# Performance work log

Hardware: AMD Instinct MI355X
Metric: run time of the kernel (lower is better)

The kernel has to match this reference:

```python
import jax, jax.numpy as jnp
import numpy as np


def setup_inputs() -> dict:
    key = jax.random.key(0)
    k1, k2 = jax.random.split(key)
    latents = jax.random.normal(k1, (32, 1024, 64), dtype=jnp.float32)
    codebook = jax.random.normal(k2, (8192, 64), dtype=jnp.float32)
    return {"latents": latents, "codebook": codebook}


def reference(latents, codebook):
    # Faithful to: cdist(latents_flat, codebook) -> argmin(dim=1) -> reshape(B, L)
    B, L, D = latents.shape
    x = latents.reshape(-1, D)                         # (N, D)
    x2 = jnp.sum(x * x, axis=1, keepdims=True)         # (N, 1)
    c2 = jnp.sum(codebook * codebook, axis=1)          # (K,)
    # (N, K) distance matrix, then argmin reduction
    d2 = x2 - 2.0 * (x @ codebook.T) + c2[None, :]
    indices = jnp.argmin(d2, axis=1)                   # (N,)
    return indices.reshape(B, L)
```

## Files before the change

### kernel.cpp

```cpp
#include <hip/hip_runtime.h>
#include <stdint.h>


#define N_TOTAL 32768
#define K_CODES 8192
#define EPS_GAP 0.008f

typedef __attribute__((ext_vector_type(16))) float  floatx16;
typedef __attribute__((ext_vector_type(8)))  __bf16 bf16x8;

#define O_C2    0u
#define O_CBSW  32768u
#define O_PS1   2129920u
#define O_PS2   2654208u
#define O_PI1   3178496u
#define O_CNT   3702784u
#define O_LIST  3703040u
#define O_SLOT  3834112u
#define WS_NEED 4096256u

__device__ __forceinline__ unsigned int fkey(float s) {
    unsigned int u = __float_as_uint(s);
    return (u & 0x80000000u) ? ~u : (u | 0x80000000u);
}

__device__ __forceinline__ void load_lds16(const void* g, void* l) {
    __builtin_amdgcn_global_load_lds(
        (const __attribute__((address_space(1))) unsigned int*)g,
        (__attribute__((address_space(3))) unsigned int*)l, 16, 0, 0);
}

__global__ __launch_bounds__(256) void vq_prep(
    const float4* __restrict__ cb, uint4* __restrict__ cbSw,
    float* __restrict__ c2, int* __restrict__ cnt) {
    __shared__ float red[256];
    const int m = threadIdx.x & 31, g = threadIdx.x >> 5;
    const int rb = blockIdx.x;
    if (rb == 0 && threadIdx.x == 0) *cnt = 0;
    float4 a = cb[(size_t)(rb * 32 + m) * 16 + g * 2];
    float4 b = cb[(size_t)(rb * 32 + m) * 16 + g * 2 + 1];
    float x[8] = {a.x, a.y, a.z, a.w, b.x, b.y, b.z, b.w};
    bf16x8 hv, lv;
    float ss = 0.f;
#pragma unroll
    for (int i = 0; i < 8; ++i) {
        float v  = x[i];
        __bf16 hb = (__bf16)v;
        float r  = v - (float)hb;
        hv[i] = hb;
        lv[i] = (__bf16)r;
        ss += v * v;
    }
    cbSw[(size_t)rb * 512 + g * 32 + m]       = __builtin_bit_cast(uint4, hv);
    cbSw[(size_t)rb * 512 + (8 + g) * 32 + m] = __builtin_bit_cast(uint4, lv);
    red[threadIdx.x] = ss;
    __syncthreads();
    if (threadIdx.x < 32) {
        float s = 0.f;
#pragma unroll
        for (int gg = 0; gg < 8; ++gg) s += red[threadIdx.x + 32 * gg];
        c2[rb * 32 + threadIdx.x] = s;
    }
}

__global__ __launch_bounds__(256, 2) void vq_mfma(
    const float4* __restrict__ lat, const uint4* __restrict__ cbSw,
    const float* __restrict__ c2,
    float* __restrict__ pS1, float* __restrict__ pS2, int* __restrict__ pI1) {
    __shared__ uint4 Bs[2][1024];
    const int tid = threadIdx.x;
    const int wr = tid >> 6, lane = tid & 63;
    const int m = lane & 31, h = lane >> 5;

    const int q = blockIdx.x * 128 + wr * 32 + m;
    bf16x8 aH[4], aL[4];
#pragma unroll
    for (int c = 0; c < 4; ++c) {
        float4 v0 = lat[(size_t)q * 16 + c * 4 + h * 2];
        float4 v1 = lat[(size_t)q * 16 + c * 4 + h * 2 + 1];
        float x[8] = {v0.x, v0.y, v0.z, v0.w, v1.x, v1.y, v1.z, v1.w};
#pragma unroll
        for (int j = 0; j < 8; ++j) {
            float v  = x[j];
            __bf16 hb = (__bf16)v;
            aH[c][j] = hb;
            aL[c][j] = (__bf16)(v - (float)hb);
        }
    }

    float t1[16], t2[16]; int i1[16];
#pragma unroll
    for (int r = 0; r < 16; ++r) { t1[r] = -3e38f; t2[r] = -3e38f; i1[r] = 0; }

    const int kBase = blockIdx.y * 2048;
    const uint4* srcBase = cbSw + ((size_t)(kBase >> 5) << 9);
    const int dOff = wr * 64 + lane;

#pragma unroll
    for (int i = 0; i < 4; ++i)
        load_lds16(&srcBase[256 * i + dOff], &Bs[0][wr * 64 + 256 * i]);
    float c2n0 = c2[kBase + m];
    float c2n1 = c2[kBase + 32 + m];
    __syncthreads();
    float nn0 = -0.5f * c2n0;
    float nn1 = -0.5f * c2n1;

    for (int stage = 0; stage < 32; ++stage) {
        const int cur = stage & 1;
        if (stage + 1 < 32) {
            const uint4* sp = srcBase + (size_t)(stage + 1) * 1024;
#pragma unroll
            for (int i = 0; i < 4; ++i)
                load_lds16(&sp[256 * i + dOff], &Bs[cur ^ 1][wr * 64 + 256 * i]);
            c2n0 = c2[kBase + (stage + 1) * 64 + m];
            c2n1 = c2[kBase + (stage + 1) * 64 + 32 + m];
        }

#pragma unroll
        for (int kb = 0; kb < 2; ++kb) {
            const int col = kBase + stage * 64 + kb * 32 + m;
            const float nn = kb ? nn1 : nn0;
            floatx16 acc;
#pragma unroll
            for (int r = 0; r < 16; ++r) acc[r] = nn;
#pragma unroll
            for (int c = 0; c < 4; ++c) {
                bf16x8 bH = __builtin_bit_cast(bf16x8, Bs[cur][kb * 512 + (c * 2 + h) * 32 + m]);
                bf16x8 bL = __builtin_bit_cast(bf16x8, Bs[cur][kb * 512 + (8 + c * 2 + h) * 32 + m]);
                acc = __builtin_amdgcn_mfma_f32_32x32x16_bf16(aH[c], bH, acc, 0, 0, 0);
                acc = __builtin_amdgcn_mfma_f32_32x32x16_bf16(aL[c], bH, acc, 0, 0, 0);
                acc = __builtin_amdgcn_mfma_f32_32x32x16_bf16(aH[c], bL, acc, 0, 0, 0);
            }
#pragma unroll
            for (int r = 0; r < 16; ++r) {
                float a = acc[r];
                bool gt = a > t1[r];
                t2[r] = __builtin_amdgcn_fmed3f(a, t1[r], t2[r]);
                t1[r] = fmaxf(t1[r], a);
                i1[r] = gt ? col : i1[r];
            }
        }

        __syncthreads();
        nn0 = -0.5f * c2n0;
        nn1 = -0.5f * c2n1;
    }

#pragma unroll
    for (int mask = 1; mask <= 16; mask <<= 1) {
#pragma unroll
        for (int r = 0; r < 16; ++r) {
            float o1 = __shfl_xor(t1[r], mask);
            float o2 = __shfl_xor(t2[r], mask);
            int   oi = __shfl_xor(i1[r], mask);
            float n2 = fmaxf(fmaxf(t2[r], o2), fminf(t1[r], o1));
            bool take = (o1 > t1[r]) || (o1 == t1[r] && oi < i1[r]);
            t1[r] = take ? o1 : t1[r];
            i1[r] = take ? oi : i1[r];
            t2[r] = n2;
        }
    }

    if (m == 0) {
        const int qb = blockIdx.x * 128 + wr * 32;
        const int o0 = blockIdx.y * N_TOTAL;
#pragma unroll
        for (int r = 0; r < 16; ++r) {
            int row = (r & 3) + 8 * (r >> 2) + 4 * h;
            int qq = qb + row;
            pS1[o0 + qq] = -2.f * t1[r];
            pS2[o0 + qq] = -2.f * t2[r];
            pI1[o0 + qq] = i1[r];
        }
    }
}

__global__ void vq_merge4(const float* __restrict__ pS1, const float* __restrict__ pS2,
                          const int* __restrict__ pI1, int* __restrict__ out,
                          int* __restrict__ cnt, int* __restrict__ list,
                          unsigned long long* __restrict__ slot) {
    int q = blockIdx.x * 256 + threadIdx.x;
    float g1 = 3e38f, g2 = 3e38f;
    int   gi = 0x7FFFFFFF;
#pragma unroll
    for (int p = 0; p < 4; ++p) {
        float s1p = pS1[p * N_TOTAL + q];
        float s2p = pS2[p * N_TOTAL + q];
        int   i1p = pI1[p * N_TOTAL + q];
        bool take = (s1p < g1) || (s1p == g1 && i1p < gi);
        g2 = fminf(g2, fminf(s2p, take ? g1 : s1p));
        if (take) { g1 = s1p; gi = i1p; }
    }
    out[q] = gi;
    if (g2 - g1 < EPS_GAP) {
        int e = atomicAdd(cnt, 1);
        list[e] = q;
        slot[e] = 0xFFFFFFFFFFFFFFFFull;
    }
}

__global__ __launch_bounds__(256) void vq_exact2(
    const float4* __restrict__ lat, const float4* __restrict__ cb,
    const float* __restrict__ c2, const int* __restrict__ cnt,
    const int* __restrict__ list, unsigned long long* __restrict__ slot) {
    __shared__ float qv[4][64];
    const int n = *cnt;
    const int totalChunks = n * 8;
    const int wInB = threadIdx.x >> 6;
    const int lane = threadIdx.x & 63;

    for (int base = blockIdx.x * 4; base < totalChunks; base += gridDim.x * 4) {
        const int c = base + wInB;
        const bool act = c < totalChunks;
        int e = 0, q = 0, kb = 0;
        if (act) { e = c >> 3; q = list[e]; kb = (c & 7) << 10; }
        __syncthreads();
        if (act && lane < 16) {
            float4 v = lat[(size_t)q * 16 + lane];
            *(float4*)&qv[wInB][lane * 4] = v;
        }
        __syncthreads();
        if (act) {
            float best = 3e38f; int bi = 0;
#pragma unroll 2
            for (int i = 0; i < 16; ++i) {
                const int k = kb + i * 64 + lane;
                float dot = 0.f;
#pragma unroll
                for (int d4 = 0; d4 < 16; ++d4) {
                    float4 cv = cb[(size_t)k * 16 + d4];
                    dot += qv[wInB][d4 * 4 + 0] * cv.x + qv[wInB][d4 * 4 + 1] * cv.y
                         + qv[wInB][d4 * 4 + 2] * cv.z + qv[wInB][d4 * 4 + 3] * cv.w;
                }
                float s = c2[k] - 2.f * dot;
                if (s < best) { best = s; bi = k; }
            }
            unsigned long long p = ((unsigned long long)fkey(best) << 32) | (unsigned)bi;
#pragma unroll
            for (int mask = 1; mask <= 32; mask <<= 1) {
                unsigned long long o = __shfl_xor(p, mask);
                p = o < p ? o : p;
            }
            if (lane == 0) atomicMin(&slot[e], p);
        }
    }
}

__global__ void vq_write(const int* __restrict__ cnt, const int* __restrict__ list,
                         const unsigned long long* __restrict__ slot,
                         int* __restrict__ out) {
    int t = blockIdx.x * 256 + threadIdx.x;
    if (t < *cnt) out[list[t]] = (int)(slot[t] & 0xFFFFFFFFull);
}

#define BM 128
#define BN 128
#define PAD 68

__global__ void vq_norms_fb(const float4* __restrict__ cb, float* __restrict__ c2) {
    int t = blockIdx.x * 256 + threadIdx.x;
    int r = t >> 2, p = t & 3;
    float s = 0.f;
#pragma unroll
    for (int i = 0; i < 4; ++i) {
        float4 v = cb[r * 16 + p * 4 + i];
        s += v.x * v.x + v.y * v.y + v.z * v.z + v.w * v.w;
    }
    s += __shfl_xor(s, 1);
    s += __shfl_xor(s, 2);
    if (p == 0) c2[r] = s;
}

__global__ __launch_bounds__(256) void vq_fp32(
    const float4* __restrict__ lat, const float4* __restrict__ cb,
    const float* __restrict__ c2, int ktPer,
    int* __restrict__ outIdx, float* __restrict__ partS, int* __restrict__ partI,
    int writePartial) {
    __shared__ float As[BM][PAD];
    __shared__ float Bsf[BN][PAD];
    __shared__ float c2s[BN];
    const int tid = threadIdx.x;
    const int tx = tid & 15;
    const int ty = tid >> 4;
    const int nBase = blockIdx.x * BM;
    const int kt0 = blockIdx.y * ktPer;
    const int ktN = kt0 + ktPer;
#pragma unroll
    for (int r = 0; r < 8; ++r) {
        int f = tid + 256 * r;
        int mm = f >> 4, d4 = f & 15;
        float4 v = lat[(size_t)(nBase + mm) * 16 + d4];
        *(float4*)&As[mm][d4 * 4] = v;
    }
    float best[8]; int bidx[8];
#pragma unroll
    for (int ii = 0; ii < 8; ++ii) { best[ii] = 3e38f; bidx[ii] = 0; }
    for (int kt = kt0; kt < ktN; ++kt) {
        const int kbase = kt * BN;
        __syncthreads();
#pragma unroll
        for (int r = 0; r < 8; ++r) {
            int f = tid + 256 * r;
            int k = f >> 4, d4 = f & 15;
            float4 v = cb[(size_t)(kbase + k) * 16 + d4];
            *(float4*)&Bsf[k][d4 * 4] = v;
        }
        if (tid < BN) c2s[tid] = c2[kbase + tid];
        __syncthreads();
        float acc[8][8];
#pragma unroll
        for (int ii = 0; ii < 8; ++ii)
#pragma unroll
            for (int jj = 0; jj < 8; ++jj) acc[ii][jj] = 0.f;
#pragma unroll 4
        for (int d4 = 0; d4 < 16; ++d4) {
            float4 a[8], b[8];
#pragma unroll
            for (int ii = 0; ii < 8; ++ii) a[ii] = *(const float4*)&As[tx + 16 * ii][d4 * 4];
#pragma unroll
            for (int jj = 0; jj < 8; ++jj) b[jj] = *(const float4*)&Bsf[ty + 16 * jj][d4 * 4];
#pragma unroll
            for (int ii = 0; ii < 8; ++ii)
#pragma unroll
                for (int jj = 0; jj < 8; ++jj)
                    acc[ii][jj] += a[ii].x * b[jj].x + a[ii].y * b[jj].y
                                 + a[ii].z * b[jj].z + a[ii].w * b[jj].w;
        }
#pragma unroll
        for (int jj = 0; jj < 8; ++jj) {
            int k = kbase + ty + 16 * jj;
            float cc = c2s[ty + 16 * jj];
#pragma unroll
            for (int ii = 0; ii < 8; ++ii) {
                float s = cc - 2.f * acc[ii][jj];
                if (s < best[ii]) { best[ii] = s; bidx[ii] = k; }
            }
        }
    }
    __syncthreads();
    float* redS = &As[0][0];
    int*   redI = (int*)&Bsf[0][0];
#pragma unroll
    for (int ii = 0; ii < 8; ++ii) {
        int mm = tx + 16 * ii;
        redS[ty * BM + mm] = best[ii];
        redI[ty * BM + mm] = bidx[ii];
    }
    __syncthreads();
    if (tid < BM) {
        int mm = tid;
        float bs = redS[mm]; int bi = redI[mm];
#pragma unroll
        for (int t = 1; t < 16; ++t) {
            float s = redS[t * BM + mm]; int i = redI[t * BM + mm];
            if (s < bs || (s == bs && i < bi)) { bs = s; bi = i; }
        }
        int n = nBase + mm;
        if (writePartial) { partS[blockIdx.y * N_TOTAL + n] = bs; partI[blockIdx.y * N_TOTAL + n] = bi; }
        else outIdx[n] = bi;
    }
}

__global__ void vq_merge_fb(const float* __restrict__ partS, const int* __restrict__ partI,
                            int* __restrict__ out) {
    int n = blockIdx.x * 256 + threadIdx.x;
    float s0 = partS[n], s1 = partS[N_TOTAL + n];
    int   i0 = partI[n], i1 = partI[N_TOTAL + n];
    out[n] = (s1 < s0) ? i1 : i0;
}

extern "C" void kernel_launch(void* const* d_in, const int* in_sizes, int n_in,
                              void* d_out, int out_size, void* d_ws, size_t ws_size,
                              hipStream_t stream) {
    const float4* lat = (const float4*)d_in[0];
    const float4* cb  = (const float4*)d_in[1];
    int* out = (int*)d_out;
    char* ws = (char*)d_ws;

    if (ws_size >= WS_NEED) {
        float* c2   = (float*)(ws + O_C2);
        uint4* cbSw = (uint4*)(ws + O_CBSW);
        float* pS1  = (float*)(ws + O_PS1);
        float* pS2  = (float*)(ws + O_PS2);
        int*   pI1  = (int*)(ws + O_PI1);
        int*   cnt  = (int*)(ws + O_CNT);
        int*   list = (int*)(ws + O_LIST);
        unsigned long long* slot = (unsigned long long*)(ws + O_SLOT);

        vq_prep<<<256, 256, 0, stream>>>(cb, cbSw, c2, cnt);
        vq_mfma<<<dim3(256, 4), 256, 0, stream>>>(lat, cbSw, c2, pS1, pS2, pI1);
        vq_merge4<<<128, 256, 0, stream>>>(pS1, pS2, pI1, out, cnt, list, slot);
        vq_exact2<<<1024, 256, 0, stream>>>(lat, cb, c2, cnt, list, slot);
        vq_write<<<128, 256, 0, stream>>>(cnt, list, slot, out);
    } else {
        float* c2 = (float*)ws;
        vq_norms_fb<<<128, 256, 0, stream>>>(cb, c2);
        const size_t needSplit = 32768u + 2u * N_TOTAL * 4u + 2u * N_TOTAL * 4u + 64u;
        if (ws_size >= needSplit) {
            float* partS = (float*)(ws + 32768);
            int*   partI = (int*)(ws + 32768 + 2 * N_TOTAL * 4);
            dim3 grid(N_TOTAL / BM, 2);
            vq_fp32<<<grid, 256, 0, stream>>>(lat, cb, c2, (K_CODES / BN) / 2, out, partS, partI, 1);
            vq_merge_fb<<<N_TOTAL / 256, 256, 0, stream>>>(partS, partI, out);
        } else {
            dim3 grid(N_TOTAL / BM, 1);
            vq_fp32<<<grid, 256, 0, stream>>>(lat, cb, c2, K_CODES / BN, out, nullptr, nullptr, 0);
        }
    }
}
```

Before: 223.3 us.

## Triple-buffer codebook LDS tiles and preload squared norms into shared memory

Replaces the double-buffered codebook staging with a three-buffer ring. Loads run two stages ahead, and each iteration uses a single barrier gated by a partial vmcnt wait instead of a trailing full __syncthreads. The per-block slice of codebook squared norms is loaded once into LDS, so the loop no longer issues global loads for it. The goal is to hide global-to-LDS latency behind the MFMA work and cut synchronisation stalls. The cost is more LDS per block, which may limit occupancy, plus redundant reloads of the last stage at the tail.

```diff
diff --git a/kernel.cpp b/kernel.cpp
--- a/kernel.cpp
+++ b/kernel.cpp
@@ -67,7 +67,8 @@
     const float4* __restrict__ lat, const uint4* __restrict__ cbSw,
     const float* __restrict__ c2,
     float* __restrict__ pS1, float* __restrict__ pS2, int* __restrict__ pI1) {
-    __shared__ uint4 Bs[2][1024];
+    __shared__ uint4 Bs[3][1024];
+    __shared__ float c2s[2048];
     const int tid = threadIdx.x;
     const int wr = tid >> 6, lane = tid & 63;
     const int m = lane & 31, h = lane >> 5;
@@ -96,25 +97,40 @@
     const uint4* srcBase = cbSw + ((size_t)(kBase >> 5) << 9);
     const int dOff = wr * 64 + lane;
 
+    {
+        const float4* c2p = (const float4*)(c2 + kBase);
+        float4 f0 = c2p[tid * 2];
+        float4 f1 = c2p[tid * 2 + 1];
+        *(float4*)&c2s[tid * 8]     = f0;
+        *(float4*)&c2s[tid * 8 + 4] = f1;
+    }
+    __syncthreads();
+
 #pragma unroll
     for (int i = 0; i < 4; ++i)
         load_lds16(&srcBase[256 * i + dOff], &Bs[0][wr * 64 + 256 * i]);
-    float c2n0 = c2[kBase + m];
-    float c2n1 = c2[kBase + 32 + m];
-    __syncthreads();
-    float nn0 = -0.5f * c2n0;
-    float nn1 = -0.5f * c2n1;
-
+#pragma unroll
+    for (int i = 0; i < 4; ++i)
+        load_lds16(&srcBase[1024 + 256 * i + dOff], &Bs[1][wr * 64 + 256 * i]);
+
+    int cur = 0;
     for (int stage = 0; stage < 32; ++stage) {
-        const int cur = stage & 1;
-        if (stage + 1 < 32) {
-            const uint4* sp = srcBase + (size_t)(stage + 1) * 1024;
+        __builtin_amdgcn_sched_barrier(0);
+        asm volatile("s_waitcnt vmcnt(4)" ::: "memory");
+        __builtin_amdgcn_s_barrier();
+        __builtin_amdgcn_sched_barrier(0);
+
+        {
+            int nb = cur + 2; if (nb >= 3) nb -= 3;
+            const int nxt = (stage + 2 < 32) ? (stage + 2) : 31;
+            const uint4* sp = srcBase + (size_t)nxt * 1024;
 #pragma unroll
             for (int i = 0; i < 4; ++i)
-                load_lds16(&sp[256 * i + dOff], &Bs[cur ^ 1][wr * 64 + 256 * i]);
-            c2n0 = c2[kBase + (stage + 1) * 64 + m];
-            c2n1 = c2[kBase + (stage + 1) * 64 + 32 + m];
-        }
+                load_lds16(&sp[256 * i + dOff], &Bs[nb][wr * 64 + 256 * i]);
+        }
+
+        float nn0 = -0.5f * c2s[stage * 64 + m];
+        float nn1 = -0.5f * c2s[stage * 64 + 32 + m];
 
 #pragma unroll
         for (int kb = 0; kb < 2; ++kb) {
@@ -140,11 +156,9 @@
                 i1[r] = gt ? col : i1[r];
             }
         }
-
-        __syncthreads();
-        nn0 = -0.5f * c2n0;
-        nn1 = -0.5f * c2n1;
-    }
+        if (++cur == 3) cur = 0;
+    }
+    asm volatile("s_waitcnt vmcnt(0)" ::: "memory");
 
 #pragma unroll
     for (int mask = 1; mask <= 16; mask <<= 1) {
```

Result: no change. 226.9 us (+1.6%).

## Switch codebook search MFMA to 16x16x32 tiles with LDS-staged norms

Applied to the files above, without the earlier changes.

Restructures the main distance kernel from 32x32x16 MFMA tiles (128 queries per block) to 16x16x32 tiles (64 queries per block), which doubles the grid and cuts per-thread accumulator and top-2 register state. The block's codebook norms are now staged once into shared memory instead of being reloaded from global memory every stage. The kernel also raises wave priority around the MFMA section and requests three blocks per CU instead of two. The trade-off is that each block reuses the codebook tile across fewer queries, so total LDS and codebook traffic doubles in exchange for higher occupancy and less register pressure.

```diff
diff --git a/kernel.cpp b/kernel.cpp
--- a/kernel.cpp
+++ b/kernel.cpp
@@ -6,6 +6,7 @@
 #define K_CODES 8192
 #define EPS_GAP 0.008f
 
+typedef __attribute__((ext_vector_type(4)))  float  floatx4;
 typedef __attribute__((ext_vector_type(16))) float  floatx16;
 typedef __attribute__((ext_vector_type(8)))  __bf16 bf16x8;
 
@@ -63,21 +64,22 @@
     }
 }
 
-__global__ __launch_bounds__(256, 2) void vq_mfma(
+__global__ __launch_bounds__(256, 3) void vq_mfma(
     const float4* __restrict__ lat, const uint4* __restrict__ cbSw,
     const float* __restrict__ c2,
     float* __restrict__ pS1, float* __restrict__ pS2, int* __restrict__ pI1) {
     __shared__ uint4 Bs[2][1024];
+    __shared__ float c2s[2048];
     const int tid = threadIdx.x;
     const int wr = tid >> 6, lane = tid & 63;
-    const int m = lane & 31, h = lane >> 5;
-
-    const int q = blockIdx.x * 128 + wr * 32 + m;
-    bf16x8 aH[4], aL[4];
-#pragma unroll
-    for (int c = 0; c < 4; ++c) {
-        float4 v0 = lat[(size_t)q * 16 + c * 4 + h * 2];
-        float4 v1 = lat[(size_t)q * 16 + c * 4 + h * 2 + 1];
+    const int c16 = lane & 15, h4 = lane >> 4;
+
+    const int q = blockIdx.x * 64 + wr * 16 + c16;
+    bf16x8 aH[2], aL[2];
+#pragma unroll
+    for (int c = 0; c < 2; ++c) {
+        float4 v0 = lat[(size_t)q * 16 + c * 8 + h4 * 2];
+        float4 v1 = lat[(size_t)q * 16 + c * 8 + h4 * 2 + 1];
         float x[8] = {v0.x, v0.y, v0.z, v0.w, v1.x, v1.y, v1.z, v1.w};
 #pragma unroll
         for (int j = 0; j < 8; ++j) {
@@ -88,51 +90,57 @@
         }
     }
 
-    float t1[16], t2[16]; int i1[16];
-#pragma unroll
-    for (int r = 0; r < 16; ++r) { t1[r] = -3e38f; t2[r] = -3e38f; i1[r] = 0; }
+    float t1[4], t2[4]; int i1[4];
+#pragma unroll
+    for (int r = 0; r < 4; ++r) { t1[r] = -3e38f; t2[r] = -3e38f; i1[r] = 0; }
 
     const int kBase = blockIdx.y * 2048;
     const uint4* srcBase = cbSw + ((size_t)(kBase >> 5) << 9);
-    const int dOff = wr * 64 + lane;
-
+
+    {
+        const float4* c2p = (const float4*)(c2 + kBase);
+        float4 f0 = c2p[tid * 2];
+        float4 f1 = c2p[tid * 2 + 1];
+        *(float4*)&c2s[tid * 8]     = f0;
+        *(float4*)&c2s[tid * 8 + 4] = f1;
+    }
 #pragma unroll
     for (int i = 0; i < 4; ++i)
-        load_lds16(&srcBase[256 * i + dOff], &Bs[0][wr * 64 + 256 * i]);
-    float c2n0 = c2[kBase + m];
-    float c2n1 = c2[kBase + 32 + m];
+        load_lds16(&srcBase[wr * 256 + i * 64 + lane], &Bs[0][wr * 256 + i * 64]);
     __syncthreads();
-    float nn0 = -0.5f * c2n0;
-    float nn1 = -0.5f * c2n1;
-
+
+    int cur = 0;
     for (int stage = 0; stage < 32; ++stage) {
-        const int cur = stage & 1;
         if (stage + 1 < 32) {
             const uint4* sp = srcBase + (size_t)(stage + 1) * 1024;
 #pragma unroll
             for (int i = 0; i < 4; ++i)
-                load_lds16(&sp[256 * i + dOff], &Bs[cur ^ 1][wr * 64 + 256 * i]);
-            c2n0 = c2[kBase + (stage + 1) * 64 + m];
-            c2n1 = c2[kBase + (stage + 1) * 64 + 32 + m];
-        }
-
-#pragma unroll
-        for (int kb = 0; kb < 2; ++kb) {
-            const int col = kBase + stage * 64 + kb * 32 + m;
-            const float nn = kb ? nn1 : nn0;
-            floatx16 acc;
-#pragma unroll
-            for (int r = 0; r < 16; ++r) acc[r] = nn;
-#pragma unroll
-            for (int c = 0; c < 4; ++c) {
-                bf16x8 bH = __builtin_bit_cast(bf16x8, Bs[cur][kb * 512 + (c * 2 + h) * 32 + m]);
-                bf16x8 bL = __builtin_bit_cast(bf16x8, Bs[cur][kb * 512 + (8 + c * 2 + h) * 32 + m]);
-                acc = __builtin_amdgcn_mfma_f32_32x32x16_bf16(aH[c], bH, acc, 0, 0, 0);
-                acc = __builtin_amdgcn_mfma_f32_32x32x16_bf16(aL[c], bH, acc, 0, 0, 0);
-                acc = __builtin_amdgcn_mfma_f32_32x32x16_bf16(aH[c], bL, acc, 0, 0, 0);
-            }
-#pragma unroll
-            for (int r = 0; r < 16; ++r) {
+                load_lds16(&sp[wr * 256 + i * 64 + lane],
+                           &Bs[cur ^ 1][wr * 256 + i * 64]);
+        }
+
+        const int colBase = kBase + stage * 64 + c16;
+        const int cOff    = stage * 64 + c16;
+
+        __builtin_amdgcn_s_setprio(1);
+#pragma unroll
+        for (int T = 0; T < 4; ++T) {
+            const float nn = -0.5f * c2s[cOff + T * 16];
+            const int col = colBase + T * 16;
+            const int bb = (T >> 1) * 512 + (T & 1) * 16 + c16 + h4 * 32;
+            bf16x8 bH0 = __builtin_bit_cast(bf16x8, Bs[cur][bb]);
+            bf16x8 bH1 = __builtin_bit_cast(bf16x8, Bs[cur][bb + 128]);
+            bf16x8 bL0 = __builtin_bit_cast(bf16x8, Bs[cur][bb + 256]);
+            bf16x8 bL1 = __builtin_bit_cast(bf16x8, Bs[cur][bb + 384]);
+            floatx4 acc = {nn, nn, nn, nn};
+            acc = __builtin_amdgcn_mfma_f32_16x16x32_bf16(aH[0], bH0, acc, 0, 0, 0);
+            acc = __builtin_amdgcn_mfma_f32_16x16x32_bf16(aH[1], bH1, acc, 0, 0, 0);
+            acc = __builtin_amdgcn_mfma_f32_16x16x32_bf16(aL[0], bH0, acc, 0, 0, 0);
+            acc = __builtin_amdgcn_mfma_f32_16x16x32_bf16(aL[1], bH1, acc, 0, 0, 0);
+            acc = __builtin_amdgcn_mfma_f32_16x16x32_bf16(aH[0], bL0, acc, 0, 0, 0);
+            acc = __builtin_amdgcn_mfma_f32_16x16x32_bf16(aH[1], bL1, acc, 0, 0, 0);
+#pragma unroll
+            for (int r = 0; r < 4; ++r) {
                 float a = acc[r];
                 bool gt = a > t1[r];
                 t2[r] = __builtin_amdgcn_fmed3f(a, t1[r], t2[r]);
@@ -140,16 +148,16 @@
                 i1[r] = gt ? col : i1[r];
             }
         }
+        __builtin_amdgcn_s_setprio(0);
 
         __syncthreads();
-        nn0 = -0.5f * c2n0;
-        nn1 = -0.5f * c2n1;
-    }
-
-#pragma unroll
-    for (int mask = 1; mask <= 16; mask <<= 1) {
-#pragma unroll
-        for (int r = 0; r < 16; ++r) {
+        cur ^= 1;
+    }
+
+#pragma unroll
+    for (int mask = 1; mask <= 8; mask <<= 1) {
+#pragma unroll
+        for (int r = 0; r < 4; ++r) {
             float o1 = __shfl_xor(t1[r], mask);
             float o2 = __shfl_xor(t2[r], mask);
             int   oi = __shfl_xor(i1[r], mask);
@@ -161,16 +169,14 @@
         }
     }
 
-    if (m == 0) {
-        const int qb = blockIdx.x * 128 + wr * 32;
+    if (c16 == 0) {
         const int o0 = blockIdx.y * N_TOTAL;
-#pragma unroll
-        for (int r = 0; r < 16; ++r) {
-            int row = (r & 3) + 8 * (r >> 2) + 4 * h;
-            int qq = qb + row;
-            pS1[o0 + qq] = -2.f * t1[r];
-            pS2[o0 + qq] = -2.f * t2[r];
-            pI1[o0 + qq] = i1[r];
+        const int qb = blockIdx.x * 64 + wr * 16 + h4 * 4;
+#pragma unroll
+        for (int r = 0; r < 4; ++r) {
+            pS1[o0 + qb + r] = -2.f * t1[r];
+            pS2[o0 + qb + r] = -2.f * t2[r];
+            pI1[o0 + qb + r] = i1[r];
         }
     }
 }
@@ -388,7 +394,7 @@
         unsigned long long* slot = (unsigned long long*)(ws + O_SLOT);
 
         vq_prep<<<256, 256, 0, stream>>>(cb, cbSw, c2, cnt);
-        vq_mfma<<<dim3(256, 4), 256, 0, stream>>>(lat, cbSw, c2, pS1, pS2, pI1);
+        vq_mfma<<<dim3(512, 4), 256, 0, stream>>>(lat, cbSw, c2, pS1, pS2, pI1);
         vq_merge4<<<128, 256, 0, stream>>>(pS1, pS2, pI1, out, cnt, list, slot);
         vq_exact2<<<1024, 256, 0, stream>>>(lat, cb, c2, cnt, list, slot);
         vq_write<<<128, 256, 0, stream>>>(cnt, list, slot, out);
```

Result: faster. 209.0 us (-6.4%).
